# Kernel optimization log

Measured on AMD Instinct MI355X. Metric: run time of the kernel, lower is better.

Reference implementation:

```python
import jax, jax.numpy as jnp
import numpy as np

EPS = 1e-5
V, D, S, B, H, DH, FF, LE, LD = 32000, 512, 1024, 2, 8, 64, 2048, 2, 2


def _ln(x, g, b):
    m = x.mean(-1, keepdims=True)
    v = ((x - m) ** 2).mean(-1, keepdims=True)
    return (x - m) * jax.lax.rsqrt(v + EPS) * g + b


def _mha(qi, ki, vi, wq, wk, wv, uw, ub, mask):
    # wq/wk/wv: [H, D, DH] stacked per-head no-bias projections (concat order == head order)
    q = jnp.einsum('bsd,hde->bhse', qi, wq)
    k = jnp.einsum('btd,hde->bhte', ki, wk)
    v = jnp.einsum('btd,hde->bhte', vi, wv)
    scale = float(wq.shape[-1]) ** 0.5  # FAITHFUL to source: scores are MULTIPLIED by sqrt(d_head)
    s = jnp.einsum('bhse,bhte->bhst', q, k) * scale
    s = jnp.where(mask, s, -jnp.inf)  # causal tril mask applied in every attention (incl. cross)
    a = jax.nn.softmax(s, axis=-1)
    o = jnp.einsum('bhst,bhte->bhse', a, v)
    b_, h_, s_, e_ = o.shape
    o = o.transpose(0, 2, 1, 3).reshape(b_, s_, h_ * e_)
    return o @ uw + ub


def _posenc(seq, d):
    pos = jnp.arange(seq, dtype=jnp.float32)[:, None]
    den = jnp.exp(jnp.arange(0, d, 2, dtype=jnp.float32) * (-np.log(10000.0) / d))
    pe = jnp.zeros((seq, d), jnp.float32)
    pe = pe.at[:, 0::2].set(jnp.sin(pos * den))
    pe = pe.at[:, 1::2].set(jnp.cos(pos * den))
    return pe


def _forward(tokens, emb, enc_wq, enc_wk, enc_wv, enc_uo_w, enc_uo_b,
             enc_ln1_g, enc_ln1_b, enc_ln2_g, enc_ln2_b,
             enc_ff_w1, enc_ff_b1, enc_ff_w2, enc_ff_b2,
             dec_sa_wq, dec_sa_wk, dec_sa_wv, dec_sa_uo_w, dec_sa_uo_b,
             dec_ca_wq, dec_ca_wk, dec_ca_wv, dec_ca_uo_w, dec_ca_uo_b,
             dec_ln1_g, dec_ln1_b, dec_ln2_g, dec_ln2_b, dec_ln3_g, dec_ln3_b,
             dec_ff_w1, dec_ff_b1, dec_ff_w2, dec_ff_b2,
             ln_enc_g, ln_enc_b, ln_dec_g, ln_dec_b, head_w, head_b):
    b, s = tokens.shape
    d = emb.shape[1]
    x = emb[tokens] + _posenc(s, d)  # [B, S, D]
    mask = jnp.tril(jnp.ones((s, s), bool))
    enc = jax.lax.stop_gradient(x)  # source: x.detach().clone()
    for l in range(enc_wq.shape[0]):
        h = _ln(enc, enc_ln1_g[l], enc_ln1_b[l])
        enc = enc + _mha(h, h, h, enc_wq[l], enc_wk[l], enc_wv[l], enc_uo_w[l], enc_uo_b[l], mask)
        h = _ln(enc, enc_ln2_g[l], enc_ln2_b[l])
        enc = enc + (jnp.maximum(h @ enc_ff_w1[l] + enc_ff_b1[l], 0.0) @ enc_ff_w2[l] + enc_ff_b2[l])
    enc = _ln(enc, ln_enc_g, ln_enc_b)
    for l in range(dec_sa_wq.shape[0]):
        h = _ln(x, dec_ln1_g[l], dec_ln1_b[l])
        x = x + _mha(h, h, h, dec_sa_wq[l], dec_sa_wk[l], dec_sa_wv[l], dec_sa_uo_w[l], dec_sa_uo_b[l], mask)
        h = _ln(x, dec_ln2_g[l], dec_ln2_b[l])
        x = x + _mha(h, enc, enc, dec_ca_wq[l], dec_ca_wk[l], dec_ca_wv[l], dec_ca_uo_w[l], dec_ca_uo_b[l], mask)
        h = _ln(x, dec_ln3_g[l], dec_ln3_b[l])
        x = x + (jnp.maximum(h @ dec_ff_w1[l] + dec_ff_b1[l], 0.0) @ dec_ff_w2[l] + dec_ff_b2[l])
    x = _ln(x, ln_dec_g, ln_dec_b)
    return x @ head_w + head_b  # [B, S, V]


def setup_inputs():
    key = jax.random.key(0)
    ks = iter(jax.random.split(key, 64))
    def n(shape):
        return jax.random.normal(next(ks), shape, jnp.float32) * 0.02
    return {
        'tokens': jax.random.randint(next(ks), (B, S), 0, V, jnp.int32),
        'emb': n((V, D)),
        'enc_wq': n((LE, H, D, DH)), 'enc_wk': n((LE, H, D, DH)), 'enc_wv': n((LE, H, D, DH)),
        'enc_uo_w': n((LE, D, D)), 'enc_uo_b': jnp.zeros((LE, D), jnp.float32),
        'enc_ln1_g': jnp.ones((LE, D), jnp.float32), 'enc_ln1_b': jnp.zeros((LE, D), jnp.float32),
        'enc_ln2_g': jnp.ones((LE, D), jnp.float32), 'enc_ln2_b': jnp.zeros((LE, D), jnp.float32),
        'enc_ff_w1': n((LE, D, FF)), 'enc_ff_b1': jnp.zeros((LE, FF), jnp.float32),
        'enc_ff_w2': n((LE, FF, D)), 'enc_ff_b2': jnp.zeros((LE, D), jnp.float32),
        'dec_sa_wq': n((LD, H, D, DH)), 'dec_sa_wk': n((LD, H, D, DH)), 'dec_sa_wv': n((LD, H, D, DH)),
        'dec_sa_uo_w': n((LD, D, D)), 'dec_sa_uo_b': jnp.zeros((LD, D), jnp.float32),
        'dec_ca_wq': n((LD, H, D, DH)), 'dec_ca_wk': n((LD, H, D, DH)), 'dec_ca_wv': n((LD, H, D, DH)),
        'dec_ca_uo_w': n((LD, D, D)), 'dec_ca_uo_b': jnp.zeros((LD, D), jnp.float32),
        'dec_ln1_g': jnp.ones((LD, D), jnp.float32), 'dec_ln1_b': jnp.zeros((LD, D), jnp.float32),
        'dec_ln2_g': jnp.ones((LD, D), jnp.float32), 'dec_ln2_b': jnp.zeros((LD, D), jnp.float32),
        'dec_ln3_g': jnp.ones((LD, D), jnp.float32), 'dec_ln3_b': jnp.zeros((LD, D), jnp.float32),
        'dec_ff_w1': n((LD, D, FF)), 'dec_ff_b1': jnp.zeros((LD, FF), jnp.float32),
        'dec_ff_w2': n((LD, FF, D)), 'dec_ff_b2': jnp.zeros((LD, D), jnp.float32),
        'ln_enc_g': jnp.ones((D,), jnp.float32), 'ln_enc_b': jnp.zeros((D,), jnp.float32),
        'ln_dec_g': jnp.ones((D,), jnp.float32), 'ln_dec_b': jnp.zeros((D,), jnp.float32),
        'head_w': n((D, V)), 'head_b': jnp.zeros((V,), jnp.float32),
    }


def reference(tokens, emb, enc_wq, enc_wk, enc_wv, enc_uo_w, enc_uo_b,
              enc_ln1_g, enc_ln1_b, enc_ln2_g, enc_ln2_b,
              enc_ff_w1, enc_ff_b1, enc_ff_w2, enc_ff_b2,
              dec_sa_wq, dec_sa_wk, dec_sa_wv, dec_sa_uo_w, dec_sa_uo_b,
              dec_ca_wq, dec_ca_wk, dec_ca_wv, dec_ca_uo_w, dec_ca_uo_b,
              dec_ln1_g, dec_ln1_b, dec_ln2_g, dec_ln2_b, dec_ln3_g, dec_ln3_b,
              dec_ff_w1, dec_ff_b1, dec_ff_w2, dec_ff_b2,
              ln_enc_g, ln_enc_b, ln_dec_g, ln_dec_b, head_w, head_b):
    return _forward(tokens, emb, enc_wq, enc_wk, enc_wv, enc_uo_w, enc_uo_b,
                    enc_ln1_g, enc_ln1_b, enc_ln2_g, enc_ln2_b,
                    enc_ff_w1, enc_ff_b1, enc_ff_w2, enc_ff_b2,
                    dec_sa_wq, dec_sa_wk, dec_sa_wv, dec_sa_uo_w, dec_sa_uo_b,
                    dec_ca_wq, dec_ca_wk, dec_ca_wv, dec_ca_uo_w, dec_ca_uo_b,
                    dec_ln1_g, dec_ln1_b, dec_ln2_g, dec_ln2_b, dec_ln3_g, dec_ln3_b,
                    dec_ff_w1, dec_ff_b1, dec_ff_w2, dec_ff_b2,
                    ln_enc_g, ln_enc_b, ln_dec_g, ln_dec_b, head_w, head_b)
```

## Files before the change

kernel.cpp:

```cpp
#include <hip/hip_runtime.h>
#include <cstddef>
#include <cstdint>

constexpr int Vv = 32000, Dd = 512, Ss = 1024, Bb = 2, Hh = 8, DHd = 64, FFf = 2048;
constexpr int Tt = Bb * Ss;
constexpr int QKVW = 3 * Dd;
constexpr float EPSf = 1e-5f;

typedef unsigned short ushort_t;
typedef short bf16x8 __attribute__((ext_vector_type(8)));
typedef short short4v __attribute__((ext_vector_type(4)));
typedef float f32x4 __attribute__((ext_vector_type(4)));

constexpr size_t AQKV = 0;
constexpr size_t AUO  = 4718592;
constexpr size_t AFF1 = 6291456;
constexpr size_t AFF2 = 10485760;
constexpr size_t AEND = 14680064;

__device__ __forceinline__ ushort_t f2b(float f) {
  unsigned int u = __float_as_uint(f);
  unsigned int r = (u + 0x7FFFu + ((u >> 16) & 1u)) >> 16;
  return (ushort_t)r;
}
__device__ __forceinline__ float bits2f(ushort_t u) {
  return __uint_as_float((unsigned int)u << 16);
}

__device__ __forceinline__ void gload_lds16(const void* g, void* l) {
  __builtin_amdgcn_global_load_lds(
      (const __attribute__((address_space(1))) unsigned int*)g,
      (__attribute__((address_space(3))) unsigned int*)l, 16, 0, 0);
}

__global__ __launch_bounds__(256) void prep_all_k(
    const float* __restrict__ ewq, const float* __restrict__ ewk, const float* __restrict__ ewv,
    const float* __restrict__ swq, const float* __restrict__ swk, const float* __restrict__ swv,
    const float* __restrict__ cwq, const float* __restrict__ cwk, const float* __restrict__ cwv,
    const float* __restrict__ euo, const float* __restrict__ suo, const float* __restrict__ cuo,
    const float* __restrict__ eff1, const float* __restrict__ dff1,
    const float* __restrict__ eff2, const float* __restrict__ dff2,
    ushort_t* __restrict__ arena,
    const int* __restrict__ tok, const float* __restrict__ emb,
    float* __restrict__ X, float* __restrict__ ENC,
    const float* __restrict__ headw, ushort_t* __restrict__ headDst) {
  int idx = blockIdx.x;

  if (idx >= 14336 && idx < 16384) {
    int row = idx - 14336;
    int s = row & (Ss - 1);
    int t = tok[row];
    const float* e = emb + (size_t)t * Dd;
    for (int d = threadIdx.x; d < Dd; d += 256) {
      int i = d >> 1;
      float den = expf(-(float)(2 * i) * (9.210340371976184f / 512.0f));
      float ang = (float)s * den;
      float pe = (d & 1) ? cosf(ang) : sinf(ang);
      float v = e[d] + pe;
      X[(size_t)row * Dd + d] = v;
      ENC[(size_t)row * Dd + d] = v;
    }
    return;
  }

  const float* src;
  ushort_t* dst;
  int R, C, tile;
  if (idx < 4608) {
    tile = idx & 31;
    int rest = idx >> 5;
    int h = rest & 7; rest >>= 3;
    int t = rest % 3, gl = rest / 3;
    int g = gl >> 1, l = gl & 1;
    const float* bq = (g == 0) ? ewq : (g == 1) ? swq : cwq;
    const float* bk = (g == 0) ? ewk : (g == 1) ? swk : cwk;
    const float* bv = (g == 0) ? ewv : (g == 1) ? swv : cwv;
    const float* base = (t == 0) ? bq : (t == 1) ? bk : bv;
    src = base + (size_t)l * (Hh * Dd * DHd) + (size_t)h * (Dd * DHd);
    dst = arena + AQKV + (size_t)gl * (QKVW * Dd) + ((size_t)t * Dd + h * DHd) * Dd;
    R = 512; C = 64;
  } else if (idx < 6144) {
    int i2 = idx - 4608;
    tile = i2 & 255;
    int gl = i2 >> 8;
    int g = gl >> 1, l = gl & 1;
    const float* base = (g == 0) ? euo : (g == 1) ? suo : cuo;
    src = base + (size_t)l * (Dd * Dd);
    dst = arena + AUO + (size_t)gl * (Dd * Dd);
    R = 512; C = 512;
  } else if (idx < 10240) {
    int i3 = idx - 6144;
    tile = i3 & 1023;
    int dl = i3 >> 10;
    int d = dl >> 1, l = dl & 1;
    src = (d ? dff1 : eff1) + (size_t)l * (Dd * FFf);
    dst = arena + AFF1 + (size_t)dl * (Dd * FFf);
    R = 512; C = 2048;
  } else if (idx < 14336) {
    int i4 = idx - 10240;
    tile = i4 & 1023;
    int dl = i4 >> 10;
    int d = dl >> 1, l = dl & 1;
    src = (d ? dff2 : eff2) + (size_t)l * (FFf * Dd);
    dst = arena + AFF2 + (size_t)dl * (FFf * Dd);
    R = 2048; C = 512;
  } else {
    tile = idx - 16384;
    src = headw; dst = headDst;
    R = 512; C = 32000;
  }
  int nR = R >> 5;
  int r0 = (tile % nR) * 32, c0 = (tile / nR) * 32;
  __shared__ float tb[32][33];
  int tx = threadIdx.x & 31, ty = threadIdx.x >> 5;
#pragma unroll
  for (int i = 0; i < 4; i++)
    tb[ty + i * 8][tx] = src[(size_t)(r0 + ty + i * 8) * C + c0 + tx];
  __syncthreads();
#pragma unroll
  for (int i = 0; i < 4; i++)
    dst[(size_t)(c0 + ty + i * 8) * R + r0 + tx] = f2b(tb[tx][ty + i * 8]);
}

__global__ __launch_bounds__(256) void tcast_k(const float* __restrict__ in,
                                               ushort_t* __restrict__ out,
                                               int R, int C) {
  __shared__ float t[32][33];
  int c0 = blockIdx.x * 32, r0 = blockIdx.y * 32;
  int tx = threadIdx.x & 31, ty = threadIdx.x >> 5;
#pragma unroll
  for (int i = 0; i < 4; i++)
    t[ty + i * 8][tx] = in[(size_t)(r0 + ty + i * 8) * C + c0 + tx];
  __syncthreads();
#pragma unroll
  for (int i = 0; i < 4; i++)
    out[(size_t)(c0 + ty + i * 8) * R + r0 + tx] = f2b(t[tx][ty + i * 8]);
}

__global__ __launch_bounds__(256) void ln2_k(const float* __restrict__ in0,
                                             const float* __restrict__ g0,
                                             const float* __restrict__ b0,
                                             ushort_t* __restrict__ o0,
                                             const float* __restrict__ in1,
                                             const float* __restrict__ g1,
                                             const float* __restrict__ b1,
                                             ushort_t* __restrict__ o1,
                                             int nblk0) {
  int row = blockIdx.x;
  const float* in = in0; const float* g = g0; const float* b = b0; ushort_t* out = o0;
  if (row >= nblk0) { row -= nblk0; in = in1; g = g1; b = b1; out = o1; }
  const float* x = in + (size_t)row * Dd;
  int tid = threadIdx.x;
  float v0 = x[tid], v1 = x[tid + 256];
  float s = v0 + v1, ss = v0 * v0 + v1 * v1;
  for (int o = 32; o; o >>= 1) {
    s  += __shfl_down(s, o, 64);
    ss += __shfl_down(ss, o, 64);
  }
  __shared__ float rs[4], rss[4];
  int wid = tid >> 6, lane = tid & 63;
  if (lane == 0) { rs[wid] = s; rss[wid] = ss; }
  __syncthreads();
  __shared__ float mean_s, inv_s;
  if (tid == 0) {
    float a = rs[0] + rs[1] + rs[2] + rs[3];
    float c = rss[0] + rss[1] + rss[2] + rss[3];
    float m = a / Dd;
    float var = c / Dd - m * m;
    mean_s = m;
    inv_s = rsqrtf(var + EPSf);
  }
  __syncthreads();
  float m = mean_s, inv = inv_s;
  out[(size_t)row * Dd + tid]       = f2b((v0 - m) * inv * g[tid]       + b[tid]);
  out[(size_t)row * Dd + tid + 256] = f2b((v1 - m) * inv * g[tid + 256] + b[tid + 256]);
}

__device__ __forceinline__ void block_coords(int o, int nwg, bool nmajor,
                                             int nbM, int nbN, int& bmOut, int& bnOut) {
  int q = nwg >> 3, r = nwg & 7;
  int x = o & 7, i = o >> 3;
  int l = (x < r ? x * (q + 1) : r * (q + 1) + (x - r) * q) + i;
  int mb, nb;
  if (nmajor) { mb = l % nbM; nb = l / nbM; }
  else        { nb = l % nbN; mb = l / nbN; }
  bmOut = mb; bnOut = nb;
}

struct GD {
  const ushort_t* A; const ushort_t* BT; const float* bias; const float* resid;
  void* C; int N; int K; int ldc; int nbM; int nbN; int nwg; int relu; int obf16;
};

template <int BM, int BN, int BK, bool NMAJOR>
__global__ __launch_bounds__(256) void gemm2_k(GD d0, GD d1, int nblk0) {
  constexpr int FM = BM / 32, FN = BN / 32;
  constexpr int KG = BK / 8;
  __shared__ __align__(16) ushort_t As[BM * BK];
  __shared__ __align__(16) ushort_t Bs[BN * BK];

  GD d = d0;
  int o = blockIdx.x;
  if (o >= nblk0) { d = d1; o -= nblk0; }
  int mb, nb;
  block_coords(o, d.nwg, NMAJOR, d.nbM, d.nbN, mb, nb);
  int bm = mb * BM, bn = nb * BN;
  int K = d.K, ldc = d.ldc;

  int tid = threadIdx.x;
  int lane = tid & 63, w = tid >> 6;
  int wr = w >> 1, wc = w & 1;
  f32x4 acc[FM][FN];
#pragma unroll
  for (int m = 0; m < FM; m++)
#pragma unroll
    for (int n = 0; n < FN; n++) acc[m][n] = (f32x4){0.f, 0.f, 0.f, 0.f};

  const ushort_t* aBase = d.A + (size_t)bm * K;
  const ushort_t* bBase = d.BT + (size_t)bn * K;
  int lr = lane & 15;
  int lk = (lane >> 4) * 8;

  for (int k0 = 0; k0 < K; k0 += BK) {
    __syncthreads();
#pragma unroll
    for (int it = 0; it < (BM * BK) / 2048; it++) {
      int cid = it * 256 + tid;
      int row = cid / KG, c8 = cid % KG;
      int sc8 = c8 ^ (row & 7);
      gload_lds16(aBase + (size_t)row * K + k0 + sc8 * 8, &As[cid * 8]);
    }
#pragma unroll
    for (int it = 0; it < (BN * BK) / 2048; it++) {
      int cid = it * 256 + tid;
      int row = cid / KG, c8 = cid % KG;
      int sc8 = c8 ^ (row & 7);
      gload_lds16(bBase + (size_t)row * K + k0 + sc8 * 8, &Bs[cid * 8]);
    }
    __syncthreads();
#pragma unroll
    for (int kk = 0; kk < BK; kk += 32) {
      bf16x8 af[FM], bfr[FN];
#pragma unroll
      for (int m = 0; m < FM; m++) {
        int row = wr * (BM / 2) + m * 16 + lr;
        af[m] = *(const bf16x8*)&As[row * BK + ((kk + lk) ^ ((row & 7) << 3))];
      }
#pragma unroll
      for (int n = 0; n < FN; n++) {
        int row = wc * (BN / 2) + n * 16 + lr;
        bfr[n] = *(const bf16x8*)&Bs[row * BK + ((kk + lk) ^ ((row & 7) << 3))];
      }
#pragma unroll
      for (int m = 0; m < FM; m++)
#pragma unroll
        for (int n = 0; n < FN; n++)
          acc[m][n] = __builtin_amdgcn_mfma_f32_16x16x32_bf16(af[m], bfr[n], acc[m][n], 0, 0, 0);
    }
  }

  int rowg = (lane >> 4) * 4;
#pragma unroll
  for (int m = 0; m < FM; m++) {
    int row0 = bm + wr * (BM / 2) + m * 16 + rowg;
#pragma unroll
    for (int n = 0; n < FN; n++) {
      int col = bn + wc * (BN / 2) + n * 16 + lr;
      float bv = d.bias ? d.bias[col] : 0.0f;
#pragma unroll
      for (int rr = 0; rr < 4; rr++) {
        int row = row0 + rr;
        float v = acc[m][n][rr] + bv;
        if (d.resid) v += d.resid[(size_t)row * ldc + col];
        if (d.relu)  v = fmaxf(v, 0.0f);
        if (d.obf16) ((ushort_t*)d.C)[(size_t)row * ldc + col] = f2b(v);
        else         ((float*)d.C)[(size_t)row * ldc + col] = v;
      }
    }
  }
}

__global__ __launch_bounds__(128) void fattn_k(const float* __restrict__ QKV0,
                                               ushort_t* __restrict__ AO0,
                                               const float* __restrict__ QKV1,
                                               ushort_t* __restrict__ AO1,
                                               int nblk0) {
  int bid = blockIdx.x;
  const float* QKV = QKV0; ushort_t* AO = AO0;
  if (bid >= nblk0) { bid -= nblk0; QKV = QKV1; AO = AO1; }
  int i4 = bid >> 4;
  int qt = (i4 < 16) ? (31 - i4) : (i4 - 16);
  int h  = bid & 7;
  int b  = (bid >> 3) & 1;
  int q0 = qt * 32;
  int tid = threadIdx.x;
  int lane = tid & 63, w = tid >> 6;
  int g = lane >> 4, c = lane & 15;

  __shared__ __align__(16) ushort_t Qh[32 * 64], Ql[32 * 64];
  __shared__ __align__(16) ushort_t Kh[64 * 64], Kl[64 * 64];
  __shared__ __align__(16) ushort_t VT[64 * 64];
  __shared__ __align__(16) ushort_t Ps[2][16 * 64];

  {
    int row = tid >> 2, c0 = (tid & 3) * 16;
    const float* qb = QKV + ((size_t)(b * Ss + q0 + row) * QKVW + h * DHd + c0);
#pragma unroll
    for (int ii = 0; ii < 4; ii++) {
      float4 v = *(const float4*)(qb + ii * 4);
      int col = c0 + ii * 4;
      int sc = col ^ ((row & 7) << 3);
      ushort_t h0 = f2b(v.x), h1 = f2b(v.y), h2 = f2b(v.z), h3 = f2b(v.w);
      short4v hv = {(short)h0, (short)h1, (short)h2, (short)h3};
      short4v lv = {(short)f2b(v.x - bits2f(h0)), (short)f2b(v.y - bits2f(h1)),
                    (short)f2b(v.z - bits2f(h2)), (short)f2b(v.w - bits2f(h3))};
      *(short4v*)&Qh[row * 64 + sc] = hv;
      *(short4v*)&Ql[row * 64 + sc] = lv;
    }
  }

  f32x4 Oa[4];
#pragma unroll
  for (int n = 0; n < 4; n++) Oa[n] = (f32x4){0.f, 0.f, 0.f, 0.f};
  float mrow[4] = {-INFINITY, -INFINITY, -INFINITY, -INFINITY};
  float lrow[4] = {0.f, 0.f, 0.f, 0.f};

  int nkv = (qt >> 1) + 1;
  for (int it = 0; it < nkv; it++) {
    int t0 = it * 64;
    __syncthreads();
    {
      int row = tid >> 1, c0 = (tid & 1) * 32;
      const float* kb = QKV + ((size_t)(b * Ss + t0 + row) * QKVW + Dd + h * DHd + c0);
      const float* vb = kb + Dd;
#pragma unroll
      for (int ii = 0; ii < 8; ii++) {
        float4 v = *(const float4*)(kb + ii * 4);
        int col = c0 + ii * 4;
        int sc = col ^ ((row & 7) << 3);
        ushort_t h0 = f2b(v.x), h1 = f2b(v.y), h2 = f2b(v.z), h3 = f2b(v.w);
        short4v hv = {(short)h0, (short)h1, (short)h2, (short)h3};
        short4v lv = {(short)f2b(v.x - bits2f(h0)), (short)f2b(v.y - bits2f(h1)),
                      (short)f2b(v.z - bits2f(h2)), (short)f2b(v.w - bits2f(h3))};
        *(short4v*)&Kh[row * 64 + sc] = hv;
        *(short4v*)&Kl[row * 64 + sc] = lv;
      }
#pragma unroll
      for (int ii = 0; ii < 8; ii++) {
        float4 v = *(const float4*)(vb + ii * 4);
        int e0 = c0 + ii * 4;
        VT[(e0 + 0) * 64 + (row ^ (((e0 + 0) & 7) << 3))] = f2b(v.x);
        VT[(e0 + 1) * 64 + (row ^ (((e0 + 1) & 7) << 3))] = f2b(v.y);
        VT[(e0 + 2) * 64 + (row ^ (((e0 + 2) & 7) << 3))] = f2b(v.z);
        VT[(e0 + 3) * 64 + (row ^ (((e0 + 3) & 7) << 3))] = f2b(v.w);
      }
    }
    __syncthreads();

    int arow = w * 16 + c;
    int ksw0 = (0 + g * 8) ^ ((c & 7) << 3);
    int ksw1 = (32 + g * 8) ^ ((c & 7) << 3);
    bf16x8 qh0 = *(const bf16x8*)&Qh[arow * 64 + ksw0];
    bf16x8 qh1 = *(const bf16x8*)&Qh[arow * 64 + ksw1];
    bf16x8 ql0 = *(const bf16x8*)&Ql[arow * 64 + ksw0];
    bf16x8 ql1 = *(const bf16x8*)&Ql[arow * 64 + ksw1];

    f32x4 sfr[4];
#pragma unroll
    for (int n = 0; n < 4; n++) {
      int brow = n * 16 + c;
      bf16x8 kh0 = *(const bf16x8*)&Kh[brow * 64 + ksw0];
      bf16x8 kh1 = *(const bf16x8*)&Kh[brow * 64 + ksw1];
      bf16x8 kl0 = *(const bf16x8*)&Kl[brow * 64 + ksw0];
      bf16x8 kl1 = *(const bf16x8*)&Kl[brow * 64 + ksw1];
      f32x4 a = (f32x4){0.f, 0.f, 0.f, 0.f};
      a = __builtin_amdgcn_mfma_f32_16x16x32_bf16(qh0, kl0, a, 0, 0, 0);
      a = __builtin_amdgcn_mfma_f32_16x16x32_bf16(qh1, kl1, a, 0, 0, 0);
      a = __builtin_amdgcn_mfma_f32_16x16x32_bf16(ql0, kh0, a, 0, 0, 0);
      a = __builtin_amdgcn_mfma_f32_16x16x32_bf16(ql1, kh1, a, 0, 0, 0);
      a = __builtin_amdgcn_mfma_f32_16x16x32_bf16(qh0, kh0, a, 0, 0, 0);
      a = __builtin_amdgcn_mfma_f32_16x16x32_bf16(qh1, kh1, a, 0, 0, 0);
      sfr[n] = a;
    }

#pragma unroll
    for (int n = 0; n < 4; n++) {
#pragma unroll
      for (int rr = 0; rr < 4; rr++) sfr[n][rr] *= 8.0f;
    }
    if (it == nkv - 1) {
#pragma unroll
      for (int n = 0; n < 4; n++) {
        int t = t0 + n * 16 + c;
#pragma unroll
        for (int rr = 0; rr < 4; rr++) {
          int s = q0 + w * 16 + g * 4 + rr;
          if (t > s) sfr[n][rr] = -INFINITY;
        }
      }
    }

    float pnew[4], scold[4];
#pragma unroll
    for (int rr = 0; rr < 4; rr++) {
      float tm = fmaxf(fmaxf(sfr[0][rr], sfr[1][rr]), fmaxf(sfr[2][rr], sfr[3][rr]));
      tm = fmaxf(tm, __shfl_xor(tm, 1));
      tm = fmaxf(tm, __shfl_xor(tm, 2));
      tm = fmaxf(tm, __shfl_xor(tm, 4));
      tm = fmaxf(tm, __shfl_xor(tm, 8));
      float mn = fmaxf(mrow[rr], tm);
      scold[rr] = __expf(mrow[rr] - mn);
      mrow[rr] = mn;
      pnew[rr] = mn;
    }
#pragma unroll
    for (int n = 0; n < 4; n++) {
#pragma unroll
      for (int rr = 0; rr < 4; rr++) sfr[n][rr] = __expf(sfr[n][rr] - pnew[rr]);
    }
#pragma unroll
    for (int rr = 0; rr < 4; rr++) {
      float s = sfr[0][rr] + sfr[1][rr] + sfr[2][rr] + sfr[3][rr];
      s += __shfl_xor(s, 1);
      s += __shfl_xor(s, 2);
      s += __shfl_xor(s, 4);
      s += __shfl_xor(s, 8);
      lrow[rr] = lrow[rr] * scold[rr] + s;
    }

#pragma unroll
    for (int n = 0; n < 4; n++) {
#pragma unroll
      for (int rr = 0; rr < 4; rr++) {
        int prow = g * 4 + rr;
        Ps[w][prow * 64 + ((n * 16 + c) ^ ((prow & 7) << 3))] = f2b(sfr[n][rr]);
      }
    }

#pragma unroll
    for (int n = 0; n < 4; n++) {
#pragma unroll
      for (int rr = 0; rr < 4; rr++) Oa[n][rr] *= scold[rr];
    }

    bf16x8 pa0 = *(const bf16x8*)&Ps[w][c * 64 + ksw0];
    bf16x8 pa1 = *(const bf16x8*)&Ps[w][c * 64 + ksw1];
#pragma unroll
    for (int n = 0; n < 4; n++) {
      int vrow = n * 16 + c;
      bf16x8 v0 = *(const bf16x8*)&VT[vrow * 64 + ksw0];
      bf16x8 v1 = *(const bf16x8*)&VT[vrow * 64 + ksw1];
      Oa[n] = __builtin_amdgcn_mfma_f32_16x16x32_bf16(pa0, v0, Oa[n], 0, 0, 0);
      Oa[n] = __builtin_amdgcn_mfma_f32_16x16x32_bf16(pa1, v1, Oa[n], 0, 0, 0);
    }
  }

#pragma unroll
  for (int rr = 0; rr < 4; rr++) {
    float inv = 1.0f / lrow[rr];
    int row = b * Ss + q0 + w * 16 + g * 4 + rr;
#pragma unroll
    for (int n = 0; n < 4; n++) {
      AO[(size_t)row * Dd + h * DHd + n * 16 + c] = f2b(Oa[n][rr] * inv);
    }
  }
}

static GD mkGD(const ushort_t* A, const ushort_t* BT, const float* bias,
               const float* resid, void* C, int M, int N, int K, int ldc,
               int BM, int BN, int relu, int obf16) {
  GD d;
  d.A = A; d.BT = BT; d.bias = bias; d.resid = resid; d.C = C;
  d.N = N; d.K = K; d.ldc = ldc;
  d.nbM = M / BM; d.nbN = N / BN; d.nwg = d.nbM * d.nbN;
  d.relu = relu; d.obf16 = obf16;
  return d;
}

template <int BM, int BN, int BK, bool NMAJOR>
static void gemm1(hipStream_t st, GD d) {
  gemm2_k<BM, BN, BK, NMAJOR><<<dim3(d.nwg), dim3(256), 0, st>>>(d, d, d.nwg);
}
template <int BM, int BN, int BK, bool NMAJOR>
static void gemm2(hipStream_t st, GD d0, GD d1) {
  gemm2_k<BM, BN, BK, NMAJOR><<<dim3(d0.nwg + d1.nwg), dim3(256), 0, st>>>(d0, d1, d0.nwg);
}

extern "C" void kernel_launch(void* const* d_in, const int* in_sizes, int n_in,
                              void* d_out, int out_size, void* d_ws, size_t ws_size,
                              hipStream_t stream) {
  const int*   tokens    = (const int*)d_in[0];
  const float* emb       = (const float*)d_in[1];
  const float* enc_wq    = (const float*)d_in[2];
  const float* enc_wk    = (const float*)d_in[3];
  const float* enc_wv    = (const float*)d_in[4];
  const float* enc_uo_w  = (const float*)d_in[5];
  const float* enc_uo_b  = (const float*)d_in[6];
  const float* enc_ln1_g = (const float*)d_in[7];
  const float* enc_ln1_b = (const float*)d_in[8];
  const float* enc_ln2_g = (const float*)d_in[9];
  const float* enc_ln2_b = (const float*)d_in[10];
  const float* enc_ff_w1 = (const float*)d_in[11];
  const float* enc_ff_b1 = (const float*)d_in[12];
  const float* enc_ff_w2 = (const float*)d_in[13];
  const float* enc_ff_b2 = (const float*)d_in[14];
  const float* dec_sa_wq = (const float*)d_in[15];
  const float* dec_sa_wk = (const float*)d_in[16];
  const float* dec_sa_wv = (const float*)d_in[17];
  const float* dec_sa_uo_w = (const float*)d_in[18];
  const float* dec_sa_uo_b = (const float*)d_in[19];
  const float* dec_ca_wq = (const float*)d_in[20];
  const float* dec_ca_wk = (const float*)d_in[21];
  const float* dec_ca_wv = (const float*)d_in[22];
  const float* dec_ca_uo_w = (const float*)d_in[23];
  const float* dec_ca_uo_b = (const float*)d_in[24];
  const float* dec_ln1_g = (const float*)d_in[25];
  const float* dec_ln1_b = (const float*)d_in[26];
  const float* dec_ln2_g = (const float*)d_in[27];
  const float* dec_ln2_b = (const float*)d_in[28];
  const float* dec_ln3_g = (const float*)d_in[29];
  const float* dec_ln3_b = (const float*)d_in[30];
  const float* dec_ff_w1 = (const float*)d_in[31];
  const float* dec_ff_b1 = (const float*)d_in[32];
  const float* dec_ff_w2 = (const float*)d_in[33];
  const float* dec_ff_b2 = (const float*)d_in[34];
  const float* ln_enc_g  = (const float*)d_in[35];
  const float* ln_enc_b  = (const float*)d_in[36];
  const float* ln_dec_g  = (const float*)d_in[37];
  const float* ln_dec_b  = (const float*)d_in[38];
  const float* head_w    = (const float*)d_in[39];
  const float* head_b    = (const float*)d_in[40];
  float* out = (float*)d_out;

  char* ws = (char*)d_ws;
  size_t off = 0;
  auto alloc = [&](size_t bytes) {
    void* p = ws + off;
    off += (bytes + 255) & ~(size_t)255;
    return p;
  };
  ushort_t* Hb    = (ushort_t*)alloc((size_t)Tt * Dd * 2);
  ushort_t* Hb2   = (ushort_t*)alloc((size_t)Tt * Dd * 2);
  ushort_t* ENCFb = (ushort_t*)alloc((size_t)Tt * Dd * 2);
  float*    X     = (float*)alloc((size_t)Tt * Dd * 4);
  float*    ENC   = (float*)alloc((size_t)Tt * Dd * 4);
  float*    QKV   = (float*)alloc((size_t)Tt * QKVW * 4);
  float*    QKV2  = (float*)alloc((size_t)Tt * QKVW * 4);
  ushort_t* AO    = (ushort_t*)alloc((size_t)Tt * Dd * 2);
  ushort_t* AO2   = (ushort_t*)alloc((size_t)Tt * Dd * 2);
  ushort_t* Fb    = (ushort_t*)alloc((size_t)Tt * FFf * 2);
  ushort_t* ARENA = (ushort_t*)alloc(AEND * 2);

  size_t headBytes = (size_t)Vv * Dd * 2;
  bool headInPrep = (off + headBytes) <= ws_size;
  ushort_t* BThead = headInPrep ? (ushort_t*)alloc(headBytes) : (ushort_t*)X;

  dim3 blk(256), fblk(128);
  int attnB = Bb * Hh * (Ss / 32);

  {
    int nprep = 14336 + 2048 + (headInPrep ? 16000 : 0);
    prep_all_k<<<nprep, blk, 0, stream>>>(
        enc_wq, enc_wk, enc_wv, dec_sa_wq, dec_sa_wk, dec_sa_wv,
        dec_ca_wq, dec_ca_wk, dec_ca_wv,
        enc_uo_w, dec_sa_uo_w, dec_ca_uo_w,
        enc_ff_w1, dec_ff_w1, enc_ff_w2, dec_ff_w2, ARENA,
        tokens, emb, X, ENC, head_w, headInPrep ? BThead : nullptr);
  }

  auto BTq  = [&](int gl) { return ARENA + AQKV + (size_t)gl * (QKVW * Dd); };
  auto BTu  = [&](int gl) { return ARENA + AUO  + (size_t)gl * (Dd * Dd); };
  auto BT1  = [&](int dl) { return ARENA + AFF1 + (size_t)dl * (Dd * FFf); };
  auto BT2  = [&](int dl) { return ARENA + AFF2 + (size_t)dl * (FFf * Dd); };

  ln2_k<<<2 * Tt, blk, 0, stream>>>(ENC, enc_ln1_g, enc_ln1_b, Hb,
                                    X, dec_ln1_g, dec_ln1_b, Hb2, Tt);
  gemm2<64, 128, 128, true>(stream,
      mkGD(Hb,  BTq(0), nullptr, nullptr, QKV,  Tt, QKVW, Dd, QKVW, 64, 128, 0, 0),
      mkGD(Hb2, BTq(2), nullptr, nullptr, QKV2, Tt, QKVW, Dd, QKVW, 64, 128, 0, 0));
  fattn_k<<<2 * attnB, fblk, 0, stream>>>(QKV, AO, QKV2, AO2, attnB);
  gemm2<64, 64, 128, true>(stream,
      mkGD(AO,  BTu(0), enc_uo_b,    ENC, ENC, Tt, Dd, Dd, Dd, 64, 64, 0, 0),
      mkGD(AO2, BTu(2), dec_sa_uo_b, X,   X,   Tt, Dd, Dd, Dd, 64, 64, 0, 0));
  ln2_k<<<2 * Tt, blk, 0, stream>>>(ENC, enc_ln2_g, enc_ln2_b, Hb,
                                    X, dec_ln2_g, dec_ln2_b, Hb2, Tt);
  gemm2<64, 128, 128, true>(stream,
      mkGD(Hb,  BT1(0), enc_ff_b1, nullptr, Fb,   Tt, FFf, Dd, FFf,  64, 128, 1, 1),
      mkGD(Hb2, BTq(4), nullptr,   nullptr, QKV2, Tt, Dd,  Dd, QKVW, 64, 128, 0, 0));
  gemm1<64, 64, 128, false>(stream,
      mkGD(Fb, BT2(0), enc_ff_b2, ENC, ENC, Tt, Dd, FFf, Dd, 64, 64, 0, 0));

  ln2_k<<<Tt, blk, 0, stream>>>(ENC, enc_ln1_g + Dd, enc_ln1_b + Dd, Hb,
                                ENC, enc_ln1_g + Dd, enc_ln1_b + Dd, Hb, Tt);
  gemm1<64, 128, 128, true>(stream,
      mkGD(Hb, BTq(1), nullptr, nullptr, QKV, Tt, QKVW, Dd, QKVW, 64, 128, 0, 0));
  fattn_k<<<attnB, fblk, 0, stream>>>(QKV, AO, QKV, AO, attnB);
  gemm1<64, 64, 128, true>(stream,
      mkGD(AO, BTu(1), enc_uo_b + Dd, ENC, ENC, Tt, Dd, Dd, Dd, 64, 64, 0, 0));
  ln2_k<<<Tt, blk, 0, stream>>>(ENC, enc_ln2_g + Dd, enc_ln2_b + Dd, Hb,
                                ENC, enc_ln2_g + Dd, enc_ln2_b + Dd, Hb, Tt);
  gemm1<64, 128, 128, true>(stream,
      mkGD(Hb, BT1(1), enc_ff_b1 + FFf, nullptr, Fb, Tt, FFf, Dd, FFf, 64, 128, 1, 1));
  gemm1<64, 64, 128, false>(stream,
      mkGD(Fb, BT2(1), enc_ff_b2 + Dd, ENC, ENC, Tt, Dd, FFf, Dd, 64, 64, 0, 0));

  ln2_k<<<Tt, blk, 0, stream>>>(ENC, ln_enc_g, ln_enc_b, ENCFb,
                                ENC, ln_enc_g, ln_enc_b, ENCFb, Tt);
  gemm1<64, 128, 128, true>(stream,
      mkGD(ENCFb, BTq(4) + (size_t)Dd * Dd, nullptr, nullptr, QKV2 + Dd,
           Tt, 2 * Dd, Dd, QKVW, 64, 128, 0, 0));
  fattn_k<<<attnB, fblk, 0, stream>>>(QKV2, AO2, QKV2, AO2, attnB);
  gemm1<64, 64, 128, true>(stream,
      mkGD(AO2, BTu(4), dec_ca_uo_b, X, X, Tt, Dd, Dd, Dd, 64, 64, 0, 0));
  ln2_k<<<Tt, blk, 0, stream>>>(X, dec_ln3_g, dec_ln3_b, Hb,
                                X, dec_ln3_g, dec_ln3_b, Hb, Tt);
  gemm1<64, 128, 128, true>(stream,
      mkGD(Hb, BT1(2), dec_ff_b1, nullptr, Fb, Tt, FFf, Dd, FFf, 64, 128, 1, 1));
  gemm1<64, 64, 128, false>(stream,
      mkGD(Fb, BT2(2), dec_ff_b2, X, X, Tt, Dd, FFf, Dd, 64, 64, 0, 0));

  ln2_k<<<Tt, blk, 0, stream>>>(X, dec_ln1_g + Dd, dec_ln1_b + Dd, Hb,
                                X, dec_ln1_g + Dd, dec_ln1_b + Dd, Hb, Tt);
  gemm1<64, 128, 128, true>(stream,
      mkGD(Hb, BTq(3), nullptr, nullptr, QKV, Tt, QKVW, Dd, QKVW, 64, 128, 0, 0));
  fattn_k<<<attnB, fblk, 0, stream>>>(QKV, AO, QKV, AO, attnB);
  gemm1<64, 64, 128, true>(stream,
      mkGD(AO, BTu(3), dec_sa_uo_b + Dd, X, X, Tt, Dd, Dd, Dd, 64, 64, 0, 0));
  ln2_k<<<Tt, blk, 0, stream>>>(X, dec_ln2_g + Dd, dec_ln2_b + Dd, Hb,
                                X, dec_ln2_g + Dd, dec_ln2_b + Dd, Hb, Tt);
  gemm2<64, 128, 128, true>(stream,
      mkGD(Hb,    BTq(5),                    nullptr, nullptr, QKV,      Tt, Dd,     Dd, QKVW, 64, 128, 0, 0),
      mkGD(ENCFb, BTq(5) + (size_t)Dd * Dd,  nullptr, nullptr, QKV + Dd, Tt, 2 * Dd, Dd, QKVW, 64, 128, 0, 0));
  fattn_k<<<attnB, fblk, 0, stream>>>(QKV, AO, QKV, AO, attnB);
  gemm1<64, 64, 128, true>(stream,
      mkGD(AO, BTu(5), dec_ca_uo_b + Dd, X, X, Tt, Dd, Dd, Dd, 64, 64, 0, 0));
  ln2_k<<<Tt, blk, 0, stream>>>(X, dec_ln3_g + Dd, dec_ln3_b + Dd, Hb,
                                X, dec_ln3_g + Dd, dec_ln3_b + Dd, Hb, Tt);
  gemm1<64, 128, 128, true>(stream,
      mkGD(Hb, BT1(3), dec_ff_b1 + FFf, nullptr, Fb, Tt, FFf, Dd, FFf, 64, 128, 1, 1));
  gemm1<64, 64, 128, false>(stream,
      mkGD(Fb, BT2(3), dec_ff_b2 + Dd, X, X, Tt, Dd, FFf, Dd, 64, 64, 0, 0));

  ln2_k<<<Tt, blk, 0, stream>>>(X, ln_dec_g, ln_dec_b, Hb, X, ln_dec_g, ln_dec_b, Hb, Tt);

  if (!headInPrep)
    tcast_k<<<dim3(Vv / 32, Dd / 32), blk, 0, stream>>>(head_w, BThead, Dd, Vv);
  gemm1<128, 128, 64, true>(stream,
      mkGD(Hb, BThead, head_b, nullptr, out, Tt, Vv, Dd, Vv, 128, 128, 0, 0));
}
```

Baseline: 741.3 us.

## Emit pre-split bf16 hi/lo Q/K and bf16 V from QKV GEMM epilogue

The QKV projection GEMM epilogue now writes Q and K directly as bf16 high/low split pairs and V as bf16 into separate per-tensor buffers, instead of storing fp32 QKV. The attention kernel then loads these bf16 tiles with 16-byte vector copies rather than reading fp32 and converting and splitting per tile. This halves or better the attention kernel's global read traffic and removes repeated conversion work, since K/V tiles are reread by many query blocks. It also adds s_setprio around the MFMA loops, and costs more scattered stores and an extra branch in the GEMM epilogue.

```diff
diff --git a/kernel.cpp b/kernel.cpp
--- a/kernel.cpp
+++ b/kernel.cpp
@@ -9,7 +9,6 @@
 
 typedef unsigned short ushort_t;
 typedef short bf16x8 __attribute__((ext_vector_type(8)));
-typedef short short4v __attribute__((ext_vector_type(4)));
 typedef float f32x4 __attribute__((ext_vector_type(4)));
 
 constexpr size_t AQKV = 0;
@@ -190,6 +189,8 @@
 struct GD {
   const ushort_t* A; const ushort_t* BT; const float* bias; const float* resid;
   void* C; int N; int K; int ldc; int nbM; int nbN; int nwg; int relu; int obf16;
+  ushort_t* qh; ushort_t* ql; ushort_t* kh; ushort_t* kl; ushort_t* av;
+  int amode; int segoff;
 };
 
 template <int BM, int BN, int BK, bool NMAJOR>
@@ -271,23 +272,37 @@
       for (int rr = 0; rr < 4; rr++) {
         int row = row0 + rr;
         float v = acc[m][n][rr] + bv;
-        if (d.resid) v += d.resid[(size_t)row * ldc + col];
-        if (d.relu)  v = fmaxf(v, 0.0f);
-        if (d.obf16) ((ushort_t*)d.C)[(size_t)row * ldc + col] = f2b(v);
-        else         ((float*)d.C)[(size_t)row * ldc + col] = v;
+        if (d.amode) {
+          int seg = (col >> 9) + d.segoff;
+          int cc = col & 511;
+          size_t idx = (size_t)row * Dd + cc;
+          ushort_t hi = f2b(v);
+          if (seg >= 2) {
+            d.av[idx] = hi;
+          } else {
+            ushort_t lo = f2b(v - bits2f(hi));
+            if (seg == 1) { d.kh[idx] = hi; d.kl[idx] = lo; }
+            else          { d.qh[idx] = hi; d.ql[idx] = lo; }
+          }
+        } else {
+          if (d.resid) v += d.resid[(size_t)row * ldc + col];
+          if (d.relu)  v = fmaxf(v, 0.0f);
+          if (d.obf16) ((ushort_t*)d.C)[(size_t)row * ldc + col] = f2b(v);
+          else         ((float*)d.C)[(size_t)row * ldc + col] = v;
+        }
       }
     }
   }
 }
 
-__global__ __launch_bounds__(128) void fattn_k(const float* __restrict__ QKV0,
-                                               ushort_t* __restrict__ AO0,
-                                               const float* __restrict__ QKV1,
-                                               ushort_t* __restrict__ AO1,
+struct AB { const ushort_t *qh, *ql, *kh, *kl, *vb; };
+
+__global__ __launch_bounds__(128) void fattn_k(AB a0, ushort_t* __restrict__ AO0,
+                                               AB a1, ushort_t* __restrict__ AO1,
                                                int nblk0) {
   int bid = blockIdx.x;
-  const float* QKV = QKV0; ushort_t* AO = AO0;
-  if (bid >= nblk0) { bid -= nblk0; QKV = QKV1; AO = AO1; }
+  AB ab = a0; ushort_t* AO = AO0;
+  if (bid >= nblk0) { bid -= nblk0; ab = a1; AO = AO1; }
   int i4 = bid >> 4;
   int qt = (i4 < 16) ? (31 - i4) : (i4 - 16);
   int h  = bid & 7;
@@ -304,18 +319,13 @@
 
   {
     int row = tid >> 2, c0 = (tid & 3) * 16;
-    const float* qb = QKV + ((size_t)(b * Ss + q0 + row) * QKVW + h * DHd + c0);
-#pragma unroll
-    for (int ii = 0; ii < 4; ii++) {
-      float4 v = *(const float4*)(qb + ii * 4);
-      int col = c0 + ii * 4;
+    size_t base = (size_t)(b * Ss + q0 + row) * Dd + h * DHd + c0;
+#pragma unroll
+    for (int j = 0; j < 2; j++) {
+      int col = c0 + j * 8;
       int sc = col ^ ((row & 7) << 3);
-      ushort_t h0 = f2b(v.x), h1 = f2b(v.y), h2 = f2b(v.z), h3 = f2b(v.w);
-      short4v hv = {(short)h0, (short)h1, (short)h2, (short)h3};
-      short4v lv = {(short)f2b(v.x - bits2f(h0)), (short)f2b(v.y - bits2f(h1)),
-                    (short)f2b(v.z - bits2f(h2)), (short)f2b(v.w - bits2f(h3))};
-      *(short4v*)&Qh[row * 64 + sc] = hv;
-      *(short4v*)&Ql[row * 64 + sc] = lv;
+      *(bf16x8*)&Qh[row * 64 + sc] = *(const bf16x8*)&ab.qh[base + j * 8];
+      *(bf16x8*)&Ql[row * 64 + sc] = *(const bf16x8*)&ab.ql[base + j * 8];
     }
   }
 
@@ -331,28 +341,23 @@
     __syncthreads();
     {
       int row = tid >> 1, c0 = (tid & 1) * 32;
-      const float* kb = QKV + ((size_t)(b * Ss + t0 + row) * QKVW + Dd + h * DHd + c0);
-      const float* vb = kb + Dd;
-#pragma unroll
-      for (int ii = 0; ii < 8; ii++) {
-        float4 v = *(const float4*)(kb + ii * 4);
-        int col = c0 + ii * 4;
+      size_t base = (size_t)(b * Ss + t0 + row) * Dd + h * DHd + c0;
+#pragma unroll
+      for (int j = 0; j < 4; j++) {
+        int col = c0 + j * 8;
         int sc = col ^ ((row & 7) << 3);
-        ushort_t h0 = f2b(v.x), h1 = f2b(v.y), h2 = f2b(v.z), h3 = f2b(v.w);
-        short4v hv = {(short)h0, (short)h1, (short)h2, (short)h3};
-        short4v lv = {(short)f2b(v.x - bits2f(h0)), (short)f2b(v.y - bits2f(h1)),
-                      (short)f2b(v.z - bits2f(h2)), (short)f2b(v.w - bits2f(h3))};
-        *(short4v*)&Kh[row * 64 + sc] = hv;
-        *(short4v*)&Kl[row * 64 + sc] = lv;
+        *(bf16x8*)&Kh[row * 64 + sc] = *(const bf16x8*)&ab.kh[base + j * 8];
+        *(bf16x8*)&Kl[row * 64 + sc] = *(const bf16x8*)&ab.kl[base + j * 8];
       }
 #pragma unroll
-      for (int ii = 0; ii < 8; ii++) {
-        float4 v = *(const float4*)(vb + ii * 4);
-        int e0 = c0 + ii * 4;
-        VT[(e0 + 0) * 64 + (row ^ (((e0 + 0) & 7) << 3))] = f2b(v.x);
-        VT[(e0 + 1) * 64 + (row ^ (((e0 + 1) & 7) << 3))] = f2b(v.y);
-        VT[(e0 + 2) * 64 + (row ^ (((e0 + 2) & 7) << 3))] = f2b(v.z);
-        VT[(e0 + 3) * 64 + (row ^ (((e0 + 3) & 7) << 3))] = f2b(v.w);
+      for (int j = 0; j < 4; j++) {
+        bf16x8 vv = *(const bf16x8*)&ab.vb[base + j * 8];
+        int e0 = c0 + j * 8;
+#pragma unroll
+        for (int i = 0; i < 8; i++) {
+          int e = e0 + i;
+          VT[e * 64 + (row ^ ((e & 7) << 3))] = (ushort_t)vv[i];
+        }
       }
     }
     __syncthreads();
@@ -366,6 +371,7 @@
     bf16x8 ql1 = *(const bf16x8*)&Ql[arow * 64 + ksw1];
 
     f32x4 sfr[4];
+    __builtin_amdgcn_s_setprio(1);
 #pragma unroll
     for (int n = 0; n < 4; n++) {
       int brow = n * 16 + c;
@@ -382,6 +388,7 @@
       a = __builtin_amdgcn_mfma_f32_16x16x32_bf16(qh1, kh1, a, 0, 0, 0);
       sfr[n] = a;
     }
+    __builtin_amdgcn_s_setprio(0);
 
 #pragma unroll
     for (int n = 0; n < 4; n++) {
@@ -445,6 +452,7 @@
 
     bf16x8 pa0 = *(const bf16x8*)&Ps[w][c * 64 + ksw0];
     bf16x8 pa1 = *(const bf16x8*)&Ps[w][c * 64 + ksw1];
+    __builtin_amdgcn_s_setprio(1);
 #pragma unroll
     for (int n = 0; n < 4; n++) {
       int vrow = n * 16 + c;
@@ -453,6 +461,7 @@
       Oa[n] = __builtin_amdgcn_mfma_f32_16x16x32_bf16(pa0, v0, Oa[n], 0, 0, 0);
       Oa[n] = __builtin_amdgcn_mfma_f32_16x16x32_bf16(pa1, v1, Oa[n], 0, 0, 0);
     }
+    __builtin_amdgcn_s_setprio(0);
   }
 
 #pragma unroll
@@ -469,11 +478,26 @@
 static GD mkGD(const ushort_t* A, const ushort_t* BT, const float* bias,
                const float* resid, void* C, int M, int N, int K, int ldc,
                int BM, int BN, int relu, int obf16) {
-  GD d;
+  GD d{};
   d.A = A; d.BT = BT; d.bias = bias; d.resid = resid; d.C = C;
   d.N = N; d.K = K; d.ldc = ldc;
   d.nbM = M / BM; d.nbN = N / BN; d.nwg = d.nbM * d.nbN;
   d.relu = relu; d.obf16 = obf16;
+  d.amode = 0; d.segoff = 0;
+  return d;
+}
+
+struct ABuf { ushort_t *qh, *ql, *kh, *kl, *vb; };
+
+static GD mkGDA(const ushort_t* A, const ushort_t* BT, int M, int N, int K,
+                int BM, int BN, const ABuf& ab, int segoff) {
+  GD d{};
+  d.A = A; d.BT = BT; d.bias = nullptr; d.resid = nullptr; d.C = nullptr;
+  d.N = N; d.K = K; d.ldc = Dd;
+  d.nbM = M / BM; d.nbN = N / BN; d.nwg = d.nbM * d.nbN;
+  d.relu = 0; d.obf16 = 0;
+  d.qh = ab.qh; d.ql = ab.ql; d.kh = ab.kh; d.kl = ab.kl; d.av = ab.vb;
+  d.amode = 1; d.segoff = segoff;
   return d;
 }
 
@@ -484,6 +508,11 @@
 template <int BM, int BN, int BK, bool NMAJOR>
 static void gemm2(hipStream_t st, GD d0, GD d1) {
   gemm2_k<BM, BN, BK, NMAJOR><<<dim3(d0.nwg + d1.nwg), dim3(256), 0, st>>>(d0, d1, d0.nwg);
+}
+
+static AB mkAB(const ABuf& b) {
+  AB a; a.qh = b.qh; a.ql = b.ql; a.kh = b.kh; a.kl = b.kl; a.vb = b.vb;
+  return a;
 }
 
 extern "C" void kernel_launch(void* const* d_in, const int* in_sizes, int n_in,
@@ -544,8 +573,17 @@
   ushort_t* ENCFb = (ushort_t*)alloc((size_t)Tt * Dd * 2);
   float*    X     = (float*)alloc((size_t)Tt * Dd * 4);
   float*    ENC   = (float*)alloc((size_t)Tt * Dd * 4);
-  float*    QKV   = (float*)alloc((size_t)Tt * QKVW * 4);
-  float*    QKV2  = (float*)alloc((size_t)Tt * QKVW * 4);
+  ABuf S1, S2;
+  S1.qh = (ushort_t*)alloc((size_t)Tt * Dd * 2);
+  S1.ql = (ushort_t*)alloc((size_t)Tt * Dd * 2);
+  S1.kh = (ushort_t*)alloc((size_t)Tt * Dd * 2);
+  S1.kl = (ushort_t*)alloc((size_t)Tt * Dd * 2);
+  S1.vb = (ushort_t*)alloc((size_t)Tt * Dd * 2);
+  S2.qh = (ushort_t*)alloc((size_t)Tt * Dd * 2);
+  S2.ql = (ushort_t*)alloc((size_t)Tt * Dd * 2);
+  S2.kh = (ushort_t*)alloc((size_t)Tt * Dd * 2);
+  S2.kl = (ushort_t*)alloc((size_t)Tt * Dd * 2);
+  S2.vb = (ushort_t*)alloc((size_t)Tt * Dd * 2);
   ushort_t* AO    = (ushort_t*)alloc((size_t)Tt * Dd * 2);
   ushort_t* AO2   = (ushort_t*)alloc((size_t)Tt * Dd * 2);
   ushort_t* Fb    = (ushort_t*)alloc((size_t)Tt * FFf * 2);
@@ -576,25 +614,25 @@
   ln2_k<<<2 * Tt, blk, 0, stream>>>(ENC, enc_ln1_g, enc_ln1_b, Hb,
                                     X, dec_ln1_g, dec_ln1_b, Hb2, Tt);
   gemm2<64, 128, 128, true>(stream,
-      mkGD(Hb,  BTq(0), nullptr, nullptr, QKV,  Tt, QKVW, Dd, QKVW, 64, 128, 0, 0),
-      mkGD(Hb2, BTq(2), nullptr, nullptr, QKV2, Tt, QKVW, Dd, QKVW, 64, 128, 0, 0));
-  fattn_k<<<2 * attnB, fblk, 0, stream>>>(QKV, AO, QKV2, AO2, attnB);
+      mkGDA(Hb,  BTq(0), Tt, QKVW, Dd, 64, 128, S1, 0),
+      mkGDA(Hb2, BTq(2), Tt, QKVW, Dd, 64, 128, S2, 0));
+  fattn_k<<<2 * attnB, fblk, 0, stream>>>(mkAB(S1), AO, mkAB(S2), AO2, attnB);
   gemm2<64, 64, 128, true>(stream,
       mkGD(AO,  BTu(0), enc_uo_b,    ENC, ENC, Tt, Dd, Dd, Dd, 64, 64, 0, 0),
       mkGD(AO2, BTu(2), dec_sa_uo_b, X,   X,   Tt, Dd, Dd, Dd, 64, 64, 0, 0));
   ln2_k<<<2 * Tt, blk, 0, stream>>>(ENC, enc_ln2_g, enc_ln2_b, Hb,
                                     X, dec_ln2_g, dec_ln2_b, Hb2, Tt);
   gemm2<64, 128, 128, true>(stream,
-      mkGD(Hb,  BT1(0), enc_ff_b1, nullptr, Fb,   Tt, FFf, Dd, FFf,  64, 128, 1, 1),
-      mkGD(Hb2, BTq(4), nullptr,   nullptr, QKV2, Tt, Dd,  Dd, QKVW, 64, 128, 0, 0));
+      mkGD(Hb, BT1(0), enc_ff_b1, nullptr, Fb, Tt, FFf, Dd, FFf, 64, 128, 1, 1),
+      mkGDA(Hb2, BTq(4), Tt, Dd, Dd, 64, 128, S2, 0));
   gemm1<64, 64, 128, false>(stream,
       mkGD(Fb, BT2(0), enc_ff_b2, ENC, ENC, Tt, Dd, FFf, Dd, 64, 64, 0, 0));
 
   ln2_k<<<Tt, blk, 0, stream>>>(ENC, enc_ln1_g + Dd, enc_ln1_b + Dd, Hb,
                                 ENC, enc_ln1_g + Dd, enc_ln1_b + Dd, Hb, Tt);
   gemm1<64, 128, 128, true>(stream,
-      mkGD(Hb, BTq(1), nullptr, nullptr, QKV, Tt, QKVW, Dd, QKVW, 64, 128, 0, 0));
-  fattn_k<<<attnB, fblk, 0, stream>>>(QKV, AO, QKV, AO, attnB);
+      mkGDA(Hb, BTq(1), Tt, QKVW, Dd, 64, 128, S1, 0));
+  fattn_k<<<attnB, fblk, 0, stream>>>(mkAB(S1), AO, mkAB(S1), AO, attnB);
   gemm1<64, 64, 128, true>(stream,
       mkGD(AO, BTu(1), enc_uo_b + Dd, ENC, ENC, Tt, Dd, Dd, Dd, 64, 64, 0, 0));
   ln2_k<<<Tt, blk, 0, stream>>>(ENC, enc_ln2_g + Dd, enc_ln2_b + Dd, Hb,
@@ -607,9 +645,8 @@
   ln2_k<<<Tt, blk, 0, stream>>>(ENC, ln_enc_g, ln_enc_b, ENCFb,
                                 ENC, ln_enc_g, ln_enc_b, ENCFb, Tt);
   gemm1<64, 128, 128, true>(stream,
-      mkGD(ENCFb, BTq(4) + (size_t)Dd * Dd, nullptr, nullptr, QKV2 + Dd,
-           Tt, 2 * Dd, Dd, QKVW, 64, 128, 0, 0));
-  fattn_k<<<attnB, fblk, 0, stream>>>(QKV2, AO2, QKV2, AO2, attnB);
+      mkGDA(ENCFb, BTq(4) + (size_t)Dd * Dd, Tt, 2 * Dd, Dd, 64, 128, S2, 1));
+  fattn_k<<<attnB, fblk, 0, stream>>>(mkAB(S2), AO2, mkAB(S2), AO2, attnB);
   gemm1<64, 64, 128, true>(stream,
       mkGD(AO2, BTu(4), dec_ca_uo_b, X, X, Tt, Dd, Dd, Dd, 64, 64, 0, 0));
   ln2_k<<<Tt, blk, 0, stream>>>(X, dec_ln3_g, dec_ln3_b, Hb,
@@ -622,16 +659,16 @@
   ln2_k<<<Tt, blk, 0, stream>>>(X, dec_ln1_g + Dd, dec_ln1_b + Dd, Hb,
                                 X, dec_ln1_g + Dd, dec_ln1_b + Dd, Hb, Tt);
   gemm1<64, 128, 128, true>(stream,
-      mkGD(Hb, BTq(3), nullptr, nullptr, QKV, Tt, QKVW, Dd, QKVW, 64, 128, 0, 0));
-  fattn_k<<<attnB, fblk, 0, stream>>>(QKV, AO, QKV, AO, attnB);
+      mkGDA(Hb, BTq(3), Tt, QKVW, Dd, 64, 128, S1, 0));
+  fattn_k<<<attnB, fblk, 0, stream>>>(mkAB(S1), AO, mkAB(S1), AO, attnB);
   gemm1<64, 64, 128, true>(stream,
       mkGD(AO, BTu(3), dec_sa_uo_b + Dd, X, X, Tt, Dd, Dd, Dd, 64, 64, 0, 0));
   ln2_k<<<Tt, blk, 0, stream>>>(X, dec_ln2_g + Dd, dec_ln2_b + Dd, Hb,
                                 X, dec_ln2_g + Dd, dec_ln2_b + Dd, Hb, Tt);
   gemm2<64, 128, 128, true>(stream,
-      mkGD(Hb,    BTq(5),                    nullptr, nullptr, QKV,      Tt, Dd,     Dd, QKVW, 64, 128, 0, 0),
-      mkGD(ENCFb, BTq(5) + (size_t)Dd * Dd,  nullptr, nullptr, QKV + Dd, Tt, 2 * Dd, Dd, QKVW, 64, 128, 0, 0));
-  fattn_k<<<attnB, fblk, 0, stream>>>(QKV, AO, QKV, AO, attnB);
+      mkGDA(Hb,    BTq(5),                   Tt, Dd,     Dd, 64, 128, S1, 0),
+      mkGDA(ENCFb, BTq(5) + (size_t)Dd * Dd, Tt, 2 * Dd, Dd, 64, 128, S1, 1));
+  fattn_k<<<attnB, fblk, 0, stream>>>(mkAB(S1), AO, mkAB(S1), AO, attnB);
   gemm1<64, 64, 128, true>(stream,
       mkGD(AO, BTu(5), dec_ca_uo_b + Dd, X, X, Tt, Dd, Dd, Dd, 64, 64, 0, 0));
   ln2_k<<<Tt, blk, 0, stream>>>(X, dec_ln3_g + Dd, dec_ln3_b + Dd, Hb,
```

New measurement: 690.7 us. 1.07x faster.
